# Optimization experiments

Hardware: AMD Instinct MI355X
Metric: run time of the kernel (lower is better)

The kernel has to match this reference:

```python
import jax, jax.numpy as jnp
import numpy as np

N_NODES = 100000
N_EDGES = 1600000
D_FEAT = 128

def setup_inputs() -> dict:
    key = jax.random.key(0)
    k1, k2, k3 = jax.random.split(key, 3)
    h = jax.random.normal(k1, (N_NODES, D_FEAT), dtype=jnp.float32)
    src = jax.random.randint(k2, (N_EDGES,), 0, N_NODES, dtype=jnp.int64)
    dst = jax.random.randint(k3, (N_EDGES,), 0, N_NODES, dtype=jnp.int64)
    return {"h": h, "src": src, "dst": dst}

def reference(h, src, dst):
    # u_dot_v: per-edge dot product of source and destination node features.
    # score[e] = sum_d h[src[e], d] * h[dst[e], d]
    return jnp.einsum("ed,ed->e", h[src], h[dst])
```

## Files before the change

### kernel.cpp

```cpp
#include <hip/hip_runtime.h>


#define D_FEAT 128

__device__ __forceinline__ int dot4_i8(unsigned a, unsigned b, int c) {
#if __has_builtin(__builtin_amdgcn_sdot4)
    return __builtin_amdgcn_sdot4((int)a, (int)b, c, false);
#else
    int r = c;
#pragma unroll
    for (int i = 0; i < 4; ++i) {
        int ai = (int)(a << (24 - 8 * i)) >> 24;
        int bi = (int)(b << (24 - 8 * i)) >> 24;
        r += ai * bi;
    }
    return r;
#endif
}

__device__ __forceinline__ unsigned pack4(int b0, int b1, int b2, int b3) {
    return (unsigned)(b0 & 0xff) | ((unsigned)(b1 & 0xff) << 8) |
           ((unsigned)(b2 & 0xff) << 16) | ((unsigned)(b3 & 0xff) << 24);
}

__global__ __launch_bounds__(256) void quantize_rows(
    const float* __restrict__ h,
    signed char* __restrict__ q,
    float* __restrict__ scale,
    int n_rows)
{
    int tid  = blockIdx.x * blockDim.x + threadIdx.x;
    int row  = tid >> 4;
    int lane = tid & 15;
    if (row >= n_rows) return;

    const float4* p = (const float4*)(h + (long)row * D_FEAT) + lane * 2;
    float4 x = p[0];
    float4 y = p[1];

    float m = fabsf(x.x);
    m = fmaxf(m, fabsf(x.y)); m = fmaxf(m, fabsf(x.z)); m = fmaxf(m, fabsf(x.w));
    m = fmaxf(m, fabsf(y.x)); m = fmaxf(m, fabsf(y.y));
    m = fmaxf(m, fabsf(y.z)); m = fmaxf(m, fabsf(y.w));

    m = fmaxf(m, __shfl_xor(m, 8));
    m = fmaxf(m, __shfl_xor(m, 4));
    m = fmaxf(m, __shfl_xor(m, 2));
    m = fmaxf(m, __shfl_xor(m, 1));

    float inv = (m > 0.f) ? (127.f / m) : 0.f;

    int b0 = (int)rintf(x.x * inv), b1 = (int)rintf(x.y * inv);
    int b2 = (int)rintf(x.z * inv), b3 = (int)rintf(x.w * inv);
    int b4 = (int)rintf(y.x * inv), b5 = (int)rintf(y.y * inv);
    int b6 = (int)rintf(y.z * inv), b7 = (int)rintf(y.w * inv);

    uint2 o;
    o.x = pack4(b0, b1, b2, b3);
    o.y = pack4(b4, b5, b6, b7);
    ((uint2*)(q + (long)row * D_FEAT))[lane] = o;

    if (lane == 0) scale[row] = m * (1.f / 127.f);
}

__global__ __launch_bounds__(256) void edge_dot_i8_b4(
    const signed char* __restrict__ q,
    const float* __restrict__ scale,
    const int* __restrict__ src,
    const int* __restrict__ dst,
    float* __restrict__ out,
    int n_edges)
{
    int tid  = blockIdx.x * blockDim.x + threadIdx.x;
    int sub  = tid >> 3;
    int lane = tid & 7;
    int e0   = sub * 4;
    if (e0 >= n_edges) return;

    int e1 = min(e0 + 1, n_edges - 1);
    int e2 = min(e0 + 2, n_edges - 1);
    int e3 = min(e0 + 3, n_edges - 1);

    int s0 = src[e0], s1 = src[e1], s2 = src[e2], s3 = src[e3];
    int d0 = dst[e0], d1 = dst[e1], d2 = dst[e2], d3 = dst[e3];

    uint4 qa0 = ((const uint4*)(q + (long)s0 * D_FEAT))[lane];
    uint4 qa1 = ((const uint4*)(q + (long)s1 * D_FEAT))[lane];
    uint4 qa2 = ((const uint4*)(q + (long)s2 * D_FEAT))[lane];
    uint4 qa3 = ((const uint4*)(q + (long)s3 * D_FEAT))[lane];
    uint4 qb0 = ((const uint4*)(q + (long)d0 * D_FEAT))[lane];
    uint4 qb1 = ((const uint4*)(q + (long)d1 * D_FEAT))[lane];
    uint4 qb2 = ((const uint4*)(q + (long)d2 * D_FEAT))[lane];
    uint4 qb3 = ((const uint4*)(q + (long)d3 * D_FEAT))[lane];

    float fs0 = scale[s0] * scale[d0];
    float fs1 = scale[s1] * scale[d1];
    float fs2 = scale[s2] * scale[d2];
    float fs3 = scale[s3] * scale[d3];

    int i0 = dot4_i8(qa0.x, qb0.x, 0);
    i0 = dot4_i8(qa0.y, qb0.y, i0);
    i0 = dot4_i8(qa0.z, qb0.z, i0);
    i0 = dot4_i8(qa0.w, qb0.w, i0);

    int i1 = dot4_i8(qa1.x, qb1.x, 0);
    i1 = dot4_i8(qa1.y, qb1.y, i1);
    i1 = dot4_i8(qa1.z, qb1.z, i1);
    i1 = dot4_i8(qa1.w, qb1.w, i1);

    int i2 = dot4_i8(qa2.x, qb2.x, 0);
    i2 = dot4_i8(qa2.y, qb2.y, i2);
    i2 = dot4_i8(qa2.z, qb2.z, i2);
    i2 = dot4_i8(qa2.w, qb2.w, i2);

    int i3 = dot4_i8(qa3.x, qb3.x, 0);
    i3 = dot4_i8(qa3.y, qb3.y, i3);
    i3 = dot4_i8(qa3.z, qb3.z, i3);
    i3 = dot4_i8(qa3.w, qb3.w, i3);

    i0 += __shfl_xor(i0, 4); i0 += __shfl_xor(i0, 2); i0 += __shfl_xor(i0, 1);
    i1 += __shfl_xor(i1, 4); i1 += __shfl_xor(i1, 2); i1 += __shfl_xor(i1, 1);
    i2 += __shfl_xor(i2, 4); i2 += __shfl_xor(i2, 2); i2 += __shfl_xor(i2, 1);
    i3 += __shfl_xor(i3, 4); i3 += __shfl_xor(i3, 2); i3 += __shfl_xor(i3, 1);

    if (lane == 0) {
        out[e0] = (float)i0 * fs0;
        if (e0 + 1 < n_edges) out[e0 + 1] = (float)i1 * fs1;
        if (e0 + 2 < n_edges) out[e0 + 2] = (float)i2 * fs2;
        if (e0 + 3 < n_edges) out[e0 + 3] = (float)i3 * fs3;
    }
}

__global__ __launch_bounds__(256) void edge_dot_f32(
    const float* __restrict__ h,
    const int* __restrict__ src,
    const int* __restrict__ dst,
    float* __restrict__ out,
    int n_edges)
{
    int tid  = blockIdx.x * blockDim.x + threadIdx.x;
    int e    = tid >> 4;
    int lane = tid & 15;
    if (e >= n_edges) return;

    long srow = (long)src[e] * D_FEAT;
    long drow = (long)dst[e] * D_FEAT;

    const float4* hs = (const float4*)(h + srow) + lane * 2;
    const float4* hd = (const float4*)(h + drow) + lane * 2;
    float4 a0 = hs[0], a1 = hs[1], b0 = hd[0], b1 = hd[1];

    float acc = a0.x * b0.x + a0.y * b0.y + a0.z * b0.z + a0.w * b0.w
              + a1.x * b1.x + a1.y * b1.y + a1.z * b1.z + a1.w * b1.w;

    acc += __shfl_xor(acc, 8);
    acc += __shfl_xor(acc, 4);
    acc += __shfl_xor(acc, 2);
    acc += __shfl_xor(acc, 1);

    if (lane == 0) out[e] = acc;
}

extern "C" void kernel_launch(void* const* d_in, const int* in_sizes, int n_in,
                              void* d_out, int out_size, void* d_ws, size_t ws_size,
                              hipStream_t stream)
{
    const float* h   = (const float*)d_in[0];
    const int*   src = (const int*)d_in[1];
    const int*   dst = (const int*)d_in[2];
    float*       out = (float*)d_out;

    int n_edges = in_sizes[1];
    int n_feat  = in_sizes[0];
    int n_rows  = n_feat / D_FEAT;

    size_t q_sz   = (size_t)n_feat;
    size_t sc_off = (q_sz + 255) & ~(size_t)255;
    size_t need   = sc_off + (size_t)n_rows * sizeof(float);

    int block = 256;

    if (ws_size >= need) {
        signed char* q     = (signed char*)d_ws;
        float*       scale = (float*)((char*)d_ws + sc_off);

        int grid_quant = (n_rows * 16 + block - 1) / block;
        int n_sub      = (n_edges + 3) / 4;
        int grid_dot   = (n_sub * 8 + block - 1) / block;

        quantize_rows<<<grid_quant, block, 0, stream>>>(h, q, scale, n_rows);
        edge_dot_i8_b4<<<grid_dot, block, 0, stream>>>(q, scale, src, dst, out, n_edges);
    } else {
        int grid_dot = (n_edges * 16 + block - 1) / block;
        edge_dot_f32<<<grid_dot, block, 0, stream>>>(h, src, dst, out, n_edges);
    }
}
```

Before: 137.4 us.

## Split int8 feature table into halves and run two edge-dot passes

Quantization now writes the low and high 64-byte halves of each row into two separate arrays. The edge dot product runs as two passes, one per half, and the second pass adds its partial result to the output. Each half-table is 6.4 MB, so the random gathers in each pass touch a smaller working set that may stay better cached. In exchange, the src/dst indices and scales are read twice, the output is written and read back, and an extra kernel launch is added.

```diff
diff --git a/kernel.cpp b/kernel.cpp
--- a/kernel.cpp
+++ b/kernel.cpp
@@ -23,9 +23,10 @@
            ((unsigned)(b2 & 0xff) << 16) | ((unsigned)(b3 & 0xff) << 24);
 }
 
-__global__ __launch_bounds__(256) void quantize_rows(
+__global__ __launch_bounds__(256) void quantize_rows_split(
     const float* __restrict__ h,
-    signed char* __restrict__ q,
+    signed char* __restrict__ q_lo,
+    signed char* __restrict__ q_hi,
     float* __restrict__ scale,
     int n_rows)
 {
@@ -58,18 +59,23 @@
     uint2 o;
     o.x = pack4(b0, b1, b2, b3);
     o.y = pack4(b4, b5, b6, b7);
-    ((uint2*)(q + (long)row * D_FEAT))[lane] = o;
+
+    signed char* dstp = (lane < 8)
+        ? (q_lo + (long)row * 64 + (long)lane * 8)
+        : (q_hi + (long)row * 64 + (long)(lane - 8) * 8);
+    *(uint2*)dstp = o;
 
     if (lane == 0) scale[row] = m * (1.f / 127.f);
 }
 
-__global__ __launch_bounds__(256) void edge_dot_i8_b4(
-    const signed char* __restrict__ q,
+__global__ __launch_bounds__(256) void edge_dot_i8_half(
+    const signed char* __restrict__ qh,
     const float* __restrict__ scale,
     const int* __restrict__ src,
     const int* __restrict__ dst,
     float* __restrict__ out,
-    int n_edges)
+    int n_edges,
+    int accumulate)
 {
     int tid  = blockIdx.x * blockDim.x + threadIdx.x;
     int sub  = tid >> 3;
@@ -84,39 +90,29 @@
     int s0 = src[e0], s1 = src[e1], s2 = src[e2], s3 = src[e3];
     int d0 = dst[e0], d1 = dst[e1], d2 = dst[e2], d3 = dst[e3];
 
-    uint4 qa0 = ((const uint4*)(q + (long)s0 * D_FEAT))[lane];
-    uint4 qa1 = ((const uint4*)(q + (long)s1 * D_FEAT))[lane];
-    uint4 qa2 = ((const uint4*)(q + (long)s2 * D_FEAT))[lane];
-    uint4 qa3 = ((const uint4*)(q + (long)s3 * D_FEAT))[lane];
-    uint4 qb0 = ((const uint4*)(q + (long)d0 * D_FEAT))[lane];
-    uint4 qb1 = ((const uint4*)(q + (long)d1 * D_FEAT))[lane];
-    uint4 qb2 = ((const uint4*)(q + (long)d2 * D_FEAT))[lane];
-    uint4 qb3 = ((const uint4*)(q + (long)d3 * D_FEAT))[lane];
+    const uint2* qb = (const uint2*)qh;
+    uint2 a0 = qb[(long)s0 * 8 + lane];
+    uint2 a1 = qb[(long)s1 * 8 + lane];
+    uint2 a2 = qb[(long)s2 * 8 + lane];
+    uint2 a3 = qb[(long)s3 * 8 + lane];
+    uint2 b0 = qb[(long)d0 * 8 + lane];
+    uint2 b1 = qb[(long)d1 * 8 + lane];
+    uint2 b2 = qb[(long)d2 * 8 + lane];
+    uint2 b3 = qb[(long)d3 * 8 + lane];
 
     float fs0 = scale[s0] * scale[d0];
     float fs1 = scale[s1] * scale[d1];
     float fs2 = scale[s2] * scale[d2];
     float fs3 = scale[s3] * scale[d3];
 
-    int i0 = dot4_i8(qa0.x, qb0.x, 0);
-    i0 = dot4_i8(qa0.y, qb0.y, i0);
-    i0 = dot4_i8(qa0.z, qb0.z, i0);
-    i0 = dot4_i8(qa0.w, qb0.w, i0);
-
-    int i1 = dot4_i8(qa1.x, qb1.x, 0);
-    i1 = dot4_i8(qa1.y, qb1.y, i1);
-    i1 = dot4_i8(qa1.z, qb1.z, i1);
-    i1 = dot4_i8(qa1.w, qb1.w, i1);
-
-    int i2 = dot4_i8(qa2.x, qb2.x, 0);
-    i2 = dot4_i8(qa2.y, qb2.y, i2);
-    i2 = dot4_i8(qa2.z, qb2.z, i2);
-    i2 = dot4_i8(qa2.w, qb2.w, i2);
-
-    int i3 = dot4_i8(qa3.x, qb3.x, 0);
-    i3 = dot4_i8(qa3.y, qb3.y, i3);
-    i3 = dot4_i8(qa3.z, qb3.z, i3);
-    i3 = dot4_i8(qa3.w, qb3.w, i3);
+    int i0 = dot4_i8(a0.x, b0.x, 0);
+    i0 = dot4_i8(a0.y, b0.y, i0);
+    int i1 = dot4_i8(a1.x, b1.x, 0);
+    i1 = dot4_i8(a1.y, b1.y, i1);
+    int i2 = dot4_i8(a2.x, b2.x, 0);
+    i2 = dot4_i8(a2.y, b2.y, i2);
+    int i3 = dot4_i8(a3.x, b3.x, 0);
+    i3 = dot4_i8(a3.y, b3.y, i3);
 
     i0 += __shfl_xor(i0, 4); i0 += __shfl_xor(i0, 2); i0 += __shfl_xor(i0, 1);
     i1 += __shfl_xor(i1, 4); i1 += __shfl_xor(i1, 2); i1 += __shfl_xor(i1, 1);
@@ -124,10 +120,20 @@
     i3 += __shfl_xor(i3, 4); i3 += __shfl_xor(i3, 2); i3 += __shfl_xor(i3, 1);
 
     if (lane == 0) {
-        out[e0] = (float)i0 * fs0;
-        if (e0 + 1 < n_edges) out[e0 + 1] = (float)i1 * fs1;
-        if (e0 + 2 < n_edges) out[e0 + 2] = (float)i2 * fs2;
-        if (e0 + 3 < n_edges) out[e0 + 3] = (float)i3 * fs3;
+        float v0 = (float)i0 * fs0;
+        float v1 = (float)i1 * fs1;
+        float v2 = (float)i2 * fs2;
+        float v3 = (float)i3 * fs3;
+        if (accumulate) {
+            v0 += out[e0];
+            if (e0 + 1 < n_edges) v1 += out[e0 + 1];
+            if (e0 + 2 < n_edges) v2 += out[e0 + 2];
+            if (e0 + 3 < n_edges) v3 += out[e0 + 3];
+        }
+        out[e0] = v0;
+        if (e0 + 1 < n_edges) out[e0 + 1] = v1;
+        if (e0 + 2 < n_edges) out[e0 + 2] = v2;
+        if (e0 + 3 < n_edges) out[e0 + 3] = v3;
     }
 }
 
@@ -174,22 +180,25 @@
     int n_feat  = in_sizes[0];
     int n_rows  = n_feat / D_FEAT;
 
-    size_t q_sz   = (size_t)n_feat;
-    size_t sc_off = (q_sz + 255) & ~(size_t)255;
-    size_t need   = sc_off + (size_t)n_rows * sizeof(float);
+    size_t half_sz = (size_t)n_rows * 64;
+    size_t sc_off  = (2 * half_sz + 255) & ~(size_t)255;
+    size_t need    = sc_off + (size_t)n_rows * sizeof(float);
 
     int block = 256;
 
     if (ws_size >= need) {
-        signed char* q     = (signed char*)d_ws;
+        signed char* q_lo  = (signed char*)d_ws;
+        signed char* q_hi  = (signed char*)d_ws + half_sz;
         float*       scale = (float*)((char*)d_ws + sc_off);
 
         int grid_quant = (n_rows * 16 + block - 1) / block;
         int n_sub      = (n_edges + 3) / 4;
-        int grid_dot   = (n_sub * 8 + block - 1) / block;
-
-        quantize_rows<<<grid_quant, block, 0, stream>>>(h, q, scale, n_rows);
-        edge_dot_i8_b4<<<grid_dot, block, 0, stream>>>(q, scale, src, dst, out, n_edges);
+        long threads   = (long)n_sub * 8;
+        int grid_dot   = (int)((threads + block - 1) / block);
+
+        quantize_rows_split<<<grid_quant, block, 0, stream>>>(h, q_lo, q_hi, scale, n_rows);
+        edge_dot_i8_half<<<grid_dot, block, 0, stream>>>(q_lo, scale, src, dst, out, n_edges, 0);
+        edge_dot_i8_half<<<grid_dot, block, 0, stream>>>(q_hi, scale, src, dst, out, n_edges, 1);
     } else {
         int grid_dot = (n_edges * 16 + block - 1) / block;
         edge_dot_f32<<<grid_dot, block, 0, stream>>>(h, src, dst, out, n_edges);
```

Result: slower. 170.9 us (+24.4%).
